# Performance work log

Measured on AMD Instinct MI355X. Metric: run time of the kernel, lower is better.

## Reference

```python
import jax, jax.numpy as jnp
import numpy as np
import math

N_HEAD = 16
ROPE_BASE = 10000.0

def _rope_cos_sin(seq_len, head_dim, dtype):
    inv_freq = 1.0 / (ROPE_BASE ** (jnp.arange(0, head_dim, 2, dtype=jnp.float32) / head_dim))
    t = jnp.arange(seq_len, dtype=jnp.float32)
    freqs = t[:, None] * inv_freq[None, :]            # [S, D/2]
    emb = jnp.concatenate([freqs, freqs], axis=-1)     # [S, D]
    # broadcast shape [1, 1, S, D] to match q/k [B, H, S, D]
    return jnp.cos(emb)[None, None].astype(dtype), jnp.sin(emb)[None, None].astype(dtype)

def _rotate_half(x):
    x1, x2 = jnp.split(x, 2, axis=-1)
    return jnp.concatenate([-x2, x1], axis=-1)

def setup_inputs() -> dict:
    key = jax.random.key(0)
    ks = jax.random.split(key, 5)
    B, S, E = 2, 2048, 1024
    x = jax.random.normal(ks[0], (B, S, E), dtype=jnp.float32)
    init = 1.0 / math.sqrt(E)
    Wq = jax.random.normal(ks[1], (E, E), dtype=jnp.float32) * init
    Wk = jax.random.normal(ks[2], (E, E), dtype=jnp.float32) * init
    Wv = jax.random.normal(ks[3], (E, E), dtype=jnp.float32) * init
    Wo = jax.random.normal(ks[4], (E, E), dtype=jnp.float32) * init
    # causal mask: True = masked (masked_fill with -inf)
    attn_mask = jnp.triu(jnp.ones((S, S), dtype=bool), k=1)
    return {"x": x, "Wq": Wq, "Wk": Wk, "Wv": Wv, "Wo": Wo, "attn_mask": attn_mask}

def reference(x, Wq, Wk, Wv, Wo, attn_mask):
    B, S, E = x.shape
    H = N_HEAD
    D = E // H
    # projections (torch Linear: y = x @ W.T), split heads -> [B, H, S, D]
    def proj(W):
        return jnp.einsum('bse,fe->bsf', x, W).reshape(B, S, H, D).transpose(0, 2, 1, 3)
    q, k, v = proj(Wq), proj(Wk), proj(Wv)
    cos, sin = _rope_cos_sin(S, D, x.dtype)
    q = q * cos + _rotate_half(q) * sin
    k = k * cos + _rotate_half(k) * sin
    scale = 1.0 / math.sqrt(D)
    scores = jnp.einsum('bhqd,bhkd->bhqk', q, k) * scale  # [B, H, S, S]
    scores = jnp.where(attn_mask[None, None], -jnp.inf, scores)
    attn = jax.nn.softmax(scores, axis=-1)
    out = jnp.einsum('bhqk,bhkd->bhqd', attn, v)           # [B, H, S, D]
    out = out.transpose(0, 2, 1, 3).reshape(B, S, E)
    return jnp.einsum('bse,fe->bsf', out, Wo)
```

## Files before the change

### kernel.cpp

```cpp
#include <hip/hip_runtime.h>
#include <hip/hip_bf16.h>

#define NB 2
#define NH 16
#define SEQ 2048
#define HD 64
#define EMB 1024

typedef unsigned short u16;
typedef unsigned int u32;
typedef __attribute__((ext_vector_type(8))) short bf16x8;
typedef __attribute__((ext_vector_type(4))) float f32x4;
typedef __attribute__((ext_vector_type(8))) unsigned short us8;

__device__ __forceinline__ float b2f(u16 u) {
    union { unsigned int i; float f; } v; v.i = ((unsigned int)u) << 16; return v.f;
}
__device__ __forceinline__ u16 f2b(float f) {
    union { float f; unsigned int i; } v; v.f = f;
    unsigned int x = v.i;
    return (u16)((x + 0x7FFFu + ((x >> 16) & 1u)) >> 16);
}
__device__ __forceinline__ u32 pk2(float a, float b) {
    union { __hip_bfloat162 h; u32 u; } v;
    v.h = __float22bfloat162_rn(make_float2(a, b));
    return v.u;
}

__device__ __forceinline__ void gld16(const u16* g, u16* l) {
    __builtin_amdgcn_global_load_lds((const __attribute__((address_space(1))) void*)g,
                                     (__attribute__((address_space(3))) void*)l, 16, 0, 0);
}

__global__ __launch_bounds__(256)
void detect_dtype_54571854463007(const u16* __restrict__ x, int* __restrict__ flag) {
    __shared__ int cnt;
    if (threadIdx.x == 0) cnt = 0;
    __syncthreads();
    const u16 v = x[threadIdx.x];
    const int e = (v >> 7) & 0xFF;
    if (e >= 110 && e <= 135) atomicAdd(&cnt, 1);
    __syncthreads();
    if (threadIdx.x == 0) *flag = (cnt >= 200) ? 1 : 0;
}

__device__ __forceinline__ void conv8(const void* src, u16* dst, int i, int isbf16) {
    if (isbf16) {
        *reinterpret_cast<uint4*>(dst + i) =
            *reinterpret_cast<const uint4*>((const u16*)src + i);
    } else {
        const float* s = (const float*)src + i;
        float4 a = *reinterpret_cast<const float4*>(s);
        float4 b = *reinterpret_cast<const float4*>(s + 4);
        us8 v;
        v[0] = f2b(a.x); v[1] = f2b(a.y); v[2] = f2b(a.z); v[3] = f2b(a.w);
        v[4] = f2b(b.x); v[5] = f2b(b.y); v[6] = f2b(b.z); v[7] = f2b(b.w);
        *reinterpret_cast<us8*>(dst + i) = v;
    }
}

__global__ __launch_bounds__(256)
void convert_54571854463007(const void* __restrict__ src, u16* __restrict__ dst,
                            const int* __restrict__ flagp, int n) {
    const int i = (blockIdx.x * 256 + threadIdx.x) * 8;
    if (i >= n) return;
    conv8(src, dst, i, *flagp);
}

__global__ __launch_bounds__(256)
void convertw_54571854463007(const void* __restrict__ w0, const void* __restrict__ w1,
                             const void* __restrict__ w2, const void* __restrict__ w3,
                             u16* __restrict__ dqkv, u16* __restrict__ dob,
                             const int* __restrict__ flagp) {
    const int NW = EMB * EMB;
    const int seg = blockIdx.y;
    const void* src = (seg == 0) ? w0 : (seg == 1) ? w1 : (seg == 2) ? w2 : w3;
    u16* dst = (seg < 3) ? (dqkv + (size_t)seg * NW) : dob;
    const int i = (blockIdx.x * 256 + threadIdx.x) * 8;
    conv8(src, dst, i, *flagp);
}

template<int OUT_MODE>
__global__ __launch_bounds__(256)
void gemm_mfma_54571854463007(const u16* __restrict__ A, const u16* __restrict__ Bw,
                              void* __restrict__ C, const int* __restrict__ flagp,
                              int M, int N, int K) {
    __shared__ __align__(16) u16 As[128 * 32];
    __shared__ __align__(16) u16 Bs[128 * 32];
    const int tid  = threadIdx.x;
    const int wave = tid >> 6, lane = tid & 63;
    const int quad = lane >> 4, fr = lane & 15;
    const int wr = (wave >> 1) * 64, wc = (wave & 1) * 64;
    const int m0 = blockIdx.y * 128, n0 = blockIdx.x * 128;
    const int r0 = tid >> 2;
    const int kc = (tid & 3) * 8;
    const f32x4 zz = {0.f, 0.f, 0.f, 0.f};
    f32x4 acc[4][4];
#pragma unroll
    for (int i = 0; i < 4; ++i)
#pragma unroll
        for (int j = 0; j < 4; ++j) acc[i][j] = zz;

    for (int k0 = 0; k0 < K; k0 += 32) {
        gld16(A  + (size_t)(m0 + r0) * K + k0 + kc,      &As[wave * 512]);
        gld16(A  + (size_t)(m0 + 64 + r0) * K + k0 + kc, &As[2048 + wave * 512]);
        gld16(Bw + (size_t)(n0 + r0) * K + k0 + kc,      &Bs[wave * 512]);
        gld16(Bw + (size_t)(n0 + 64 + r0) * K + k0 + kc, &Bs[2048 + wave * 512]);
        __syncthreads();
        bf16x8 af[4], bfr[4];
#pragma unroll
        for (int mi = 0; mi < 4; ++mi)
            af[mi] = *reinterpret_cast<const bf16x8*>(&As[(wr + mi * 16 + fr) * 32 + quad * 8]);
#pragma unroll
        for (int ni = 0; ni < 4; ++ni)
            bfr[ni] = *reinterpret_cast<const bf16x8*>(&Bs[(wc + ni * 16 + fr) * 32 + quad * 8]);
#pragma unroll
        for (int mi = 0; mi < 4; ++mi)
#pragma unroll
            for (int ni = 0; ni < 4; ++ni)
                acc[mi][ni] = __builtin_amdgcn_mfma_f32_16x16x32_bf16(af[mi], bfr[ni], acc[mi][ni], 0, 0, 0);
        __syncthreads();
    }

    if (OUT_MODE == 1) {
        const int t0 = n0 >> 10;
        if (t0 == 0) {
            const float SCL = 0.18033688011112042f;
#pragma unroll
            for (int mi = 0; mi < 4; ++mi)
#pragma unroll
                for (int ni = 0; ni < 4; ++ni)
#pragma unroll
                    for (int r = 0; r < 4; ++r) acc[mi][ni][r] *= SCL;
        }
        if (t0 < 2) {
            const float inv0 = __powf(10000.f, -(float)fr / 32.f);
            const float inv1 = __powf(10000.f, -(float)(fr + 16) / 32.f);
#pragma unroll
            for (int mi = 0; mi < 4; ++mi)
#pragma unroll
                for (int r = 0; r < 4; ++r) {
                    const int s = (m0 + wr + mi * 16 + quad * 4 + r) & (SEQ - 1);
#pragma unroll
                    for (int nl = 0; nl < 2; ++nl) {
                        float sn, cs;
                        __sincosf((float)s * (nl ? inv1 : inv0), &sn, &cs);
                        const float lo = acc[mi][nl][r], hi = acc[mi][nl + 2][r];
                        acc[mi][nl][r]     = lo * cs - hi * sn;
                        acc[mi][nl + 2][r] = hi * cs + lo * sn;
                    }
                }
        }
    }

    const int isbf16 = (OUT_MODE == 0) ? *flagp : 0;
    const size_t TS = (size_t)NB * NH * SEQ * HD;
#pragma unroll
    for (int mi = 0; mi < 4; ++mi)
#pragma unroll
        for (int ni = 0; ni < 4; ++ni)
#pragma unroll
            for (int r = 0; r < 4; ++r) {
                const int m = m0 + wr + mi * 16 + quad * 4 + r;
                const int n = n0 + wc + ni * 16 + fr;
                const float v = acc[mi][ni][r];
                if (OUT_MODE == 1) {
                    const int t = n >> 10, idx = n & 1023;
                    const int h = idx >> 6, d = idx & 63;
                    const int b = m >> 11, s = m & (SEQ - 1);
                    ((u16*)C)[t * TS + ((((size_t)b * NH + h) * SEQ + s) << 6) + d] = f2b(v);
                } else {
                    if (isbf16) ((u16*)C)[(size_t)m * N + n] = f2b(v);
                    else        ((float*)C)[(size_t)m * N + n] = v;
                }
            }
}

__device__ __forceinline__ void loadK_54571854463007(const u16* Kt, int fr, int quad,
                                                     bf16x8* kc) {
#pragma unroll
    for (int nt = 0; nt < 4; ++nt) {
        const u16* kp = Kt + (size_t)(nt * 16 + fr) * HD + quad * 8;
        kc[2 * nt]     = *reinterpret_cast<const bf16x8*>(kp);
        kc[2 * nt + 1] = *reinterpret_cast<const bf16x8*>(kp + 32);
    }
}

__global__ __launch_bounds__(256)
void flash_54571854463007(const u16* __restrict__ Q, const u16* __restrict__ K,
                          const u16* __restrict__ V, u16* __restrict__ AO) {
    __shared__ __align__(16) u16 Vt[2 * 4608];
    __shared__ __align__(16) u16 Ps[4608];
    const int tid  = threadIdx.x;
    const int w    = tid >> 6, lane = tid & 63;
    const int quad = lane >> 4, fr = lane & 15;
    const int qA = blockIdx.x;
    const int qB = 31 - qA;
    const int h = blockIdx.y, b = blockIdx.z;
    const size_t base = ((size_t)b * NH + h) * SEQ * HD;
    const int k2   = (tid & 31) * 2;
    const int key0 = (k2 & 3) * 16 + (k2 >> 2);
    const int d8   = ((tid >> 5) & 7) * 8;
    const int total = 33;

    const bf16x8 ones = {(short)0x3F80, (short)0x3F80, (short)0x3F80, (short)0x3F80,
                         (short)0x3F80, (short)0x3F80, (short)0x3F80, (short)0x3F80};

    const u16* qpA = Q + base + (size_t)(qA * 64 + w * 16 + fr) * HD + quad * 8;
    const u16* qpB = Q + base + (size_t)(qB * 64 + w * 16 + fr) * HD + quad * 8;
    const bf16x8 aqA0 = *reinterpret_cast<const bf16x8*>(qpA);
    const bf16x8 aqA1 = *reinterpret_cast<const bf16x8*>(qpA + 32);
    const bf16x8 aqB0 = *reinterpret_cast<const bf16x8*>(qpB);
    const bf16x8 aqB1 = *reinterpret_cast<const bf16x8*>(qpB + 32);

    bf16x8 kc[8], kn[8];
    loadK_54571854463007(K + base, fr, quad, kc);
    us8 vc0, vc1, vn0, vn1;
    {
        const u16* vs = V + base + (size_t)key0 * HD + d8;
        vc0 = *reinterpret_cast<const us8*>(vs);
        vc1 = *reinterpret_cast<const us8*>(vs + 16 * HD);
    }

    const f32x4 zz = {0.f, 0.f, 0.f, 0.f};
    f32x4 lacc = zz;
    f32x4 oacc[4];
#pragma unroll
    for (int nt = 0; nt < 4; ++nt) oacc[nt] = zz;

    for (int j = 0; j < total; ++j) {
        const int buf   = j & 1;
        const int phase = (j > qA) ? 1 : 0;
        const int qtile = phase ? qB : qA;
        const int kt    = phase ? (j - qA - 1) : j;
        const int vbase = buf * 4608;
#pragma unroll
        for (int jj = 0; jj < 8; ++jj) {
            const u32 pk = ((u32)(u16)vc1[jj] << 16) | (u32)(u16)vc0[jj];
            *reinterpret_cast<u32*>(&Vt[vbase + (d8 + jj) * 72 + k2]) = pk;
        }
        __syncthreads();
        if (j + 1 < total) {
            const int nkt = (j + 1 > qA) ? (j - qA) : (j + 1);
            loadK_54571854463007(K + base + (size_t)nkt * 64 * HD, fr, quad, kn);
            const u16* vs = V + base + (size_t)(nkt * 64 + key0) * HD + d8;
            vn0 = *reinterpret_cast<const us8*>(vs);
            vn1 = *reinterpret_cast<const us8*>(vs + 16 * HD);
        }
        const bf16x8 a0 = phase ? aqB0 : aqA0;
        const bf16x8 a1 = phase ? aqB1 : aqA1;
        f32x4 sa[4];
#pragma unroll
        for (int nt = 0; nt < 4; ++nt) {
            sa[nt] = __builtin_amdgcn_mfma_f32_16x16x32_bf16(a0, kc[2 * nt], zz, 0, 0, 0);
            sa[nt] = __builtin_amdgcn_mfma_f32_16x16x32_bf16(a1, kc[2 * nt + 1], sa[nt], 0, 0, 0);
        }
        if (kt == qtile) {
#pragma unroll
            for (int nt = 0; nt < 4; ++nt)
#pragma unroll
                for (int r = 0; r < 4; ++r)
                    if (nt * 16 + fr > w * 16 + quad * 4 + r) sa[nt][r] = -__builtin_inff();
        }
#pragma unroll
        for (int r = 0; r < 4; ++r) {
            const float p0 = exp2f(sa[0][r]);
            const float p1 = exp2f(sa[1][r]);
            const float p2 = exp2f(sa[2][r]);
            const float p3 = exp2f(sa[3][r]);
            *reinterpret_cast<uint2*>(&Ps[(w * 16 + quad * 4 + r) * 72 + 4 * fr]) =
                make_uint2(pk2(p0, p1), pk2(p2, p3));
        }
        bf16x8 ap0 = *reinterpret_cast<const bf16x8*>(&Ps[(w * 16 + fr) * 72 + quad * 8]);
        bf16x8 ap1 = *reinterpret_cast<const bf16x8*>(&Ps[(w * 16 + fr) * 72 + 32 + quad * 8]);
        lacc = __builtin_amdgcn_mfma_f32_16x16x32_bf16(ap0, ones, lacc, 0, 0, 0);
        lacc = __builtin_amdgcn_mfma_f32_16x16x32_bf16(ap1, ones, lacc, 0, 0, 0);
#pragma unroll
        for (int nt = 0; nt < 4; ++nt) {
            bf16x8 bv0 = *reinterpret_cast<const bf16x8*>(&Vt[vbase + (nt * 16 + fr) * 72 + quad * 8]);
            bf16x8 bv1 = *reinterpret_cast<const bf16x8*>(&Vt[vbase + (nt * 16 + fr) * 72 + 32 + quad * 8]);
            oacc[nt] = __builtin_amdgcn_mfma_f32_16x16x32_bf16(ap0, bv0, oacc[nt], 0, 0, 0);
            oacc[nt] = __builtin_amdgcn_mfma_f32_16x16x32_bf16(ap1, bv1, oacc[nt], 0, 0, 0);
        }
#pragma unroll
        for (int i = 0; i < 8; ++i) kc[i] = kn[i];
        vc0 = vn0; vc1 = vn1;
        if (j == qA || j == total - 1) {
#pragma unroll
            for (int r = 0; r < 4; ++r) {
                const float inv = 1.0f / lacc[r];
                const int q = qtile * 64 + w * 16 + quad * 4 + r;
#pragma unroll
                for (int nt = 0; nt < 4; ++nt)
                    AO[(((size_t)b * SEQ + q) * NH + h) * HD + nt * 16 + fr] = f2b(oacc[nt][r] * inv);
            }
            if (j == qA) {
                lacc = zz;
#pragma unroll
                for (int nt = 0; nt < 4; ++nt) oacc[nt] = zz;
            }
        }
    }
}

extern "C" void kernel_launch(void* const* d_in, const int* in_sizes, int n_in,
                              void* d_out, int out_size, void* d_ws, size_t ws_size,
                              hipStream_t stream) {
    (void)in_sizes; (void)n_in; (void)out_size; (void)ws_size;
    const void* x  = d_in[0];
    const void* Wq = d_in[1];
    const void* Wk = d_in[2];
    const void* Wv = d_in[3];
    const void* Wo = d_in[4];

    char* ws = (char*)d_ws;
    const size_t MB = 1024 * 1024;
    int* flag = (int*)ws;
    u16* xb   = (u16*)(ws + 64);
    u16* Wqkv = (u16*)(ws + 64 + 8 * MB);
    u16* Wob  = (u16*)(ws + 64 + 14 * MB);
    u16* Qb   = (u16*)(ws + 64 + 16 * MB);
    u16* Kb   = (u16*)(ws + 64 + 24 * MB);
    u16* Vb   = (u16*)(ws + 64 + 32 * MB);
    u16* AO   = xb;

    detect_dtype_54571854463007<<<1, 256, 0, stream>>>((const u16*)x, flag);

    const int NX = NB * SEQ * EMB;
    const int NW = EMB * EMB;
    convert_54571854463007<<<NX / 2048, 256, 0, stream>>>(x, xb, flag, NX);
    convertw_54571854463007<<<dim3(NW / 2048, 4), 256, 0, stream>>>(Wq, Wk, Wv, Wo, Wqkv, Wob, flag);

    const int M = NB * SEQ;
    gemm_mfma_54571854463007<1><<<dim3(3 * EMB / 128, M / 128), 256, 0, stream>>>(
        xb, Wqkv, Qb, flag, M, 3 * EMB, EMB);

    flash_54571854463007<<<dim3(16, NH, NB), 256, 0, stream>>>(Qb, Kb, Vb, AO);

    gemm_mfma_54571854463007<0><<<dim3(EMB / 128, M / 128), 256, 0, stream>>>(
        AO, Wob, d_out, flag, M, EMB, EMB);
}
```

Measured before the change: 240.4 us.

## Software-pipeline QK^T scores one tile ahead of softmax and PV in attention loop

Restructures the attention inner loop so the QK^T MFMA for tile j+1 is issued in iteration j, overlapping with the exp2/P-store and PV MFMAs of tile j. K loads are moved two tiles ahead to feed this. The aim is to hide MFMA latency and the exp/LDS dependency chain; in exchange it adds register pressure (extra score and K buffers), which could lower occupancy.

Measured after the change: 242.6 us. About the same (+0.9%).

```diff
diff --git a/kernel.cpp b/kernel.cpp
--- a/kernel.cpp
+++ b/kernel.cpp
@@ -213,16 +213,34 @@
     const bf16x8 aqB0 = *reinterpret_cast<const bf16x8*>(qpB);
     const bf16x8 aqB1 = *reinterpret_cast<const bf16x8*>(qpB + 32);
 
+    const f32x4 zz = {0.f, 0.f, 0.f, 0.f};
     bf16x8 kc[8], kn[8];
-    loadK_54571854463007(K + base, fr, quad, kc);
     us8 vc0, vc1, vn0, vn1;
+    f32x4 sa_cur[4], sa_next[4];
+
+    #define KTILE(i) (((i) <= qA) ? (i) : ((i) - qA - 1))
+
     {
+        bf16x8 k0[8];
+        loadK_54571854463007(K + base, fr, quad, k0);
         const u16* vs = V + base + (size_t)key0 * HD + d8;
         vc0 = *reinterpret_cast<const us8*>(vs);
         vc1 = *reinterpret_cast<const us8*>(vs + 16 * HD);
-    }
-
-    const f32x4 zz = {0.f, 0.f, 0.f, 0.f};
+        loadK_54571854463007(K + base + (size_t)KTILE(1) * 64 * HD, fr, quad, kc);
+#pragma unroll
+        for (int nt = 0; nt < 4; ++nt) {
+            sa_cur[nt] = __builtin_amdgcn_mfma_f32_16x16x32_bf16(aqA0, k0[2 * nt], zz, 0, 0, 0);
+            sa_cur[nt] = __builtin_amdgcn_mfma_f32_16x16x32_bf16(aqA1, k0[2 * nt + 1], sa_cur[nt], 0, 0, 0);
+        }
+        if (qA == 0) {
+#pragma unroll
+            for (int nt = 0; nt < 4; ++nt)
+#pragma unroll
+                for (int r = 0; r < 4; ++r)
+                    if (nt * 16 + fr > w * 16 + quad * 4 + r) sa_cur[nt][r] = -__builtin_inff();
+        }
+    }
+
     f32x4 lacc = zz;
     f32x4 oacc[4];
 #pragma unroll
@@ -230,9 +248,6 @@
 
     for (int j = 0; j < total; ++j) {
         const int buf   = j & 1;
-        const int phase = (j > qA) ? 1 : 0;
-        const int qtile = phase ? qB : qA;
-        const int kt    = phase ? (j - qA - 1) : j;
         const int vbase = buf * 4608;
 #pragma unroll
         for (int jj = 0; jj < 8; ++jj) {
@@ -240,34 +255,36 @@
             *reinterpret_cast<u32*>(&Vt[vbase + (d8 + jj) * 72 + k2]) = pk;
         }
         __syncthreads();
+        if (j + 2 < total)
+            loadK_54571854463007(K + base + (size_t)KTILE(j + 2) * 64 * HD, fr, quad, kn);
         if (j + 1 < total) {
-            const int nkt = (j + 1 > qA) ? (j - qA) : (j + 1);
-            loadK_54571854463007(K + base + (size_t)nkt * 64 * HD, fr, quad, kn);
-            const u16* vs = V + base + (size_t)(nkt * 64 + key0) * HD + d8;
+            const u16* vs = V + base + (size_t)(KTILE(j + 1) * 64 + key0) * HD + d8;
             vn0 = *reinterpret_cast<const us8*>(vs);
             vn1 = *reinterpret_cast<const us8*>(vs + 16 * HD);
         }
-        const bf16x8 a0 = phase ? aqB0 : aqA0;
-        const bf16x8 a1 = phase ? aqB1 : aqA1;
-        f32x4 sa[4];
-#pragma unroll
-        for (int nt = 0; nt < 4; ++nt) {
-            sa[nt] = __builtin_amdgcn_mfma_f32_16x16x32_bf16(a0, kc[2 * nt], zz, 0, 0, 0);
-            sa[nt] = __builtin_amdgcn_mfma_f32_16x16x32_bf16(a1, kc[2 * nt + 1], sa[nt], 0, 0, 0);
-        }
-        if (kt == qtile) {
-#pragma unroll
-            for (int nt = 0; nt < 4; ++nt)
-#pragma unroll
-                for (int r = 0; r < 4; ++r)
-                    if (nt * 16 + fr > w * 16 + quad * 4 + r) sa[nt][r] = -__builtin_inff();
+        if (j + 1 < total) {
+            const bool ph1 = (j + 1 > qA);
+            const bf16x8 a0 = ph1 ? aqB0 : aqA0;
+            const bf16x8 a1 = ph1 ? aqB1 : aqA1;
+#pragma unroll
+            for (int nt = 0; nt < 4; ++nt) {
+                sa_next[nt] = __builtin_amdgcn_mfma_f32_16x16x32_bf16(a0, kc[2 * nt], zz, 0, 0, 0);
+                sa_next[nt] = __builtin_amdgcn_mfma_f32_16x16x32_bf16(a1, kc[2 * nt + 1], sa_next[nt], 0, 0, 0);
+            }
+            if (j + 1 == qA || j + 1 == total - 1) {
+#pragma unroll
+                for (int nt = 0; nt < 4; ++nt)
+#pragma unroll
+                    for (int r = 0; r < 4; ++r)
+                        if (nt * 16 + fr > w * 16 + quad * 4 + r) sa_next[nt][r] = -__builtin_inff();
+            }
         }
 #pragma unroll
         for (int r = 0; r < 4; ++r) {
-            const float p0 = exp2f(sa[0][r]);
-            const float p1 = exp2f(sa[1][r]);
-            const float p2 = exp2f(sa[2][r]);
-            const float p3 = exp2f(sa[3][r]);
+            const float p0 = exp2f(sa_cur[0][r]);
+            const float p1 = exp2f(sa_cur[1][r]);
+            const float p2 = exp2f(sa_cur[2][r]);
+            const float p3 = exp2f(sa_cur[3][r]);
             *reinterpret_cast<uint2*>(&Ps[(w * 16 + quad * 4 + r) * 72 + 4 * fr]) =
                 make_uint2(pk2(p0, p1), pk2(p2, p3));
         }
@@ -283,9 +300,12 @@
             oacc[nt] = __builtin_amdgcn_mfma_f32_16x16x32_bf16(ap1, bv1, oacc[nt], 0, 0, 0);
         }
 #pragma unroll
+        for (int nt = 0; nt < 4; ++nt) sa_cur[nt] = sa_next[nt];
+#pragma unroll
         for (int i = 0; i < 8; ++i) kc[i] = kn[i];
         vc0 = vn0; vc1 = vn1;
         if (j == qA || j == total - 1) {
+            const int qtile = (j > qA) ? qB : qA;
 #pragma unroll
             for (int r = 0; r < 4; ++r) {
                 const float inv = 1.0f / lacc[r];
@@ -301,6 +321,7 @@
             }
         }
     }
+    #undef KTILE
 }
 
 extern "C" void kernel_launch(void* const* d_in, const int* in_sizes, int n_in,
```

## Split flash attention into single-wave blocks per 16-row quarter

Applied to the files above, without the earlier changes.

Launches the flash kernel as 2048 one-wave blocks, each owning a 16-row quarter of a paired causal q-tile. Each wave loads and transposes its own V tile into LDS without any block barrier, and the V double buffer and prefetch are removed. The intent is to drop __syncthreads stalls and raise occupancy with smaller LDS per block. The cost is fourfold redundant V loads and transposes, plus less latency hiding for V.

New measurement: 280.9 us. 16.9% more time.

```diff
diff --git a/kernel.cpp b/kernel.cpp
--- a/kernel.cpp
+++ b/kernel.cpp
@@ -186,41 +186,41 @@
     }
 }
 
-__global__ __launch_bounds__(256)
+__global__ __launch_bounds__(64, 2)
 void flash_54571854463007(const u16* __restrict__ Q, const u16* __restrict__ K,
                           const u16* __restrict__ V, u16* __restrict__ AO) {
-    __shared__ __align__(16) u16 Vt[2 * 4608];
-    __shared__ __align__(16) u16 Ps[4608];
-    const int tid  = threadIdx.x;
-    const int w    = tid >> 6, lane = tid & 63;
+    __shared__ __align__(16) u16 Vt[4608];
+    __shared__ __align__(16) u16 Ps[1152];
+    const int lane = threadIdx.x;
     const int quad = lane >> 4, fr = lane & 15;
-    const int qA = blockIdx.x;
-    const int qB = 31 - qA;
-    const int h = blockIdx.y, b = blockIdx.z;
+    const int lin  = blockIdx.x;
+    const int phb  = ((lin >> 5) << 3) | (lin & 7);
+    const int quarter = (lin >> 3) & 3;
+    const int p = phb & 15;
+    const int h = (phb >> 4) & 15;
+    const int b = phb >> 8;
+    const int qA = p, qB = 31 - p;
+    const int ro = quarter * 16;
     const size_t base = ((size_t)b * NH + h) * SEQ * HD;
-    const int k2   = (tid & 31) * 2;
-    const int key0 = (k2 & 3) * 16 + (k2 >> 2);
-    const int d8   = ((tid >> 5) & 7) * 8;
+    const int k2    = (lane & 31) * 2;
+    const int key0  = (k2 & 3) * 16 + (k2 >> 2);
+    const int dbase = (lane >> 5) * 32;
     const int total = 33;
 
     const bf16x8 ones = {(short)0x3F80, (short)0x3F80, (short)0x3F80, (short)0x3F80,
                          (short)0x3F80, (short)0x3F80, (short)0x3F80, (short)0x3F80};
 
-    const u16* qpA = Q + base + (size_t)(qA * 64 + w * 16 + fr) * HD + quad * 8;
-    const u16* qpB = Q + base + (size_t)(qB * 64 + w * 16 + fr) * HD + quad * 8;
+    const u16* qpA = Q + base + (size_t)(qA * 64 + ro + fr) * HD + quad * 8;
+    const u16* qpB = Q + base + (size_t)(qB * 64 + ro + fr) * HD + quad * 8;
     const bf16x8 aqA0 = *reinterpret_cast<const bf16x8*>(qpA);
     const bf16x8 aqA1 = *reinterpret_cast<const bf16x8*>(qpA + 32);
     const bf16x8 aqB0 = *reinterpret_cast<const bf16x8*>(qpB);
     const bf16x8 aqB1 = *reinterpret_cast<const bf16x8*>(qpB + 32);
 
+    #define KTILE(i) (((i) <= qA) ? (i) : ((i) - qA - 1))
+
     bf16x8 kc[8], kn[8];
     loadK_54571854463007(K + base, fr, quad, kc);
-    us8 vc0, vc1, vn0, vn1;
-    {
-        const u16* vs = V + base + (size_t)key0 * HD + d8;
-        vc0 = *reinterpret_cast<const us8*>(vs);
-        vc1 = *reinterpret_cast<const us8*>(vs + 16 * HD);
-    }
 
     const f32x4 zz = {0.f, 0.f, 0.f, 0.f};
     f32x4 lacc = zz;
@@ -229,29 +229,23 @@
     for (int nt = 0; nt < 4; ++nt) oacc[nt] = zz;
 
     for (int j = 0; j < total; ++j) {
-        const int buf   = j & 1;
-        const int phase = (j > qA) ? 1 : 0;
+        const int phase = (j > qA);
         const int qtile = phase ? qB : qA;
         const int kt    = phase ? (j - qA - 1) : j;
-        const int vbase = buf * 4608;
-#pragma unroll
-        for (int jj = 0; jj < 8; ++jj) {
-            const u32 pk = ((u32)(u16)vc1[jj] << 16) | (u32)(u16)vc0[jj];
-            *reinterpret_cast<u32*>(&Vt[vbase + (d8 + jj) * 72 + k2]) = pk;
-        }
-        __syncthreads();
-        if (j + 1 < total) {
-            const int nkt = (j + 1 > qA) ? (j - qA) : (j + 1);
-            loadK_54571854463007(K + base + (size_t)nkt * 64 * HD, fr, quad, kn);
-            const u16* vs = V + base + (size_t)(nkt * 64 + key0) * HD + d8;
-            vn0 = *reinterpret_cast<const us8*>(vs);
-            vn1 = *reinterpret_cast<const us8*>(vs + 16 * HD);
-        }
-        const bf16x8 a0 = phase ? aqB0 : aqA0;
-        const bf16x8 a1 = phase ? aqB1 : aqA1;
+        const u16* vs = V + base + (size_t)(kt * 64 + key0) * HD + dbase;
+        us8 va[4], vb[4];
+#pragma unroll
+        for (int i = 0; i < 4; ++i) {
+            va[i] = *reinterpret_cast<const us8*>(vs + i * 8);
+            vb[i] = *reinterpret_cast<const us8*>(vs + 16 * HD + i * 8);
+        }
+        if (j + 1 < total)
+            loadK_54571854463007(K + base + (size_t)KTILE(j + 1) * 64 * HD, fr, quad, kn);
         f32x4 sa[4];
 #pragma unroll
         for (int nt = 0; nt < 4; ++nt) {
+            const bf16x8 a0 = phase ? aqB0 : aqA0;
+            const bf16x8 a1 = phase ? aqB1 : aqA1;
             sa[nt] = __builtin_amdgcn_mfma_f32_16x16x32_bf16(a0, kc[2 * nt], zz, 0, 0, 0);
             sa[nt] = __builtin_amdgcn_mfma_f32_16x16x32_bf16(a1, kc[2 * nt + 1], sa[nt], 0, 0, 0);
         }
@@ -260,7 +254,7 @@
             for (int nt = 0; nt < 4; ++nt)
 #pragma unroll
                 for (int r = 0; r < 4; ++r)
-                    if (nt * 16 + fr > w * 16 + quad * 4 + r) sa[nt][r] = -__builtin_inff();
+                    if (nt * 16 + fr > ro + quad * 4 + r) sa[nt][r] = -__builtin_inff();
         }
 #pragma unroll
         for (int r = 0; r < 4; ++r) {
@@ -268,28 +262,34 @@
             const float p1 = exp2f(sa[1][r]);
             const float p2 = exp2f(sa[2][r]);
             const float p3 = exp2f(sa[3][r]);
-            *reinterpret_cast<uint2*>(&Ps[(w * 16 + quad * 4 + r) * 72 + 4 * fr]) =
+            *reinterpret_cast<uint2*>(&Ps[(quad * 4 + r) * 72 + 4 * fr]) =
                 make_uint2(pk2(p0, p1), pk2(p2, p3));
         }
-        bf16x8 ap0 = *reinterpret_cast<const bf16x8*>(&Ps[(w * 16 + fr) * 72 + quad * 8]);
-        bf16x8 ap1 = *reinterpret_cast<const bf16x8*>(&Ps[(w * 16 + fr) * 72 + 32 + quad * 8]);
+#pragma unroll
+        for (int i = 0; i < 4; ++i)
+#pragma unroll
+            for (int jj = 0; jj < 8; ++jj) {
+                const u32 pk = ((u32)(u16)vb[i][jj] << 16) | (u32)(u16)va[i][jj];
+                *reinterpret_cast<u32*>(&Vt[(dbase + i * 8 + jj) * 72 + k2]) = pk;
+            }
+        const bf16x8 ap0 = *reinterpret_cast<const bf16x8*>(&Ps[fr * 72 + quad * 8]);
+        const bf16x8 ap1 = *reinterpret_cast<const bf16x8*>(&Ps[fr * 72 + 32 + quad * 8]);
         lacc = __builtin_amdgcn_mfma_f32_16x16x32_bf16(ap0, ones, lacc, 0, 0, 0);
         lacc = __builtin_amdgcn_mfma_f32_16x16x32_bf16(ap1, ones, lacc, 0, 0, 0);
 #pragma unroll
         for (int nt = 0; nt < 4; ++nt) {
-            bf16x8 bv0 = *reinterpret_cast<const bf16x8*>(&Vt[vbase + (nt * 16 + fr) * 72 + quad * 8]);
-            bf16x8 bv1 = *reinterpret_cast<const bf16x8*>(&Vt[vbase + (nt * 16 + fr) * 72 + 32 + quad * 8]);
+            const bf16x8 bv0 = *reinterpret_cast<const bf16x8*>(&Vt[(nt * 16 + fr) * 72 + quad * 8]);
+            const bf16x8 bv1 = *reinterpret_cast<const bf16x8*>(&Vt[(nt * 16 + fr) * 72 + 32 + quad * 8]);
             oacc[nt] = __builtin_amdgcn_mfma_f32_16x16x32_bf16(ap0, bv0, oacc[nt], 0, 0, 0);
             oacc[nt] = __builtin_amdgcn_mfma_f32_16x16x32_bf16(ap1, bv1, oacc[nt], 0, 0, 0);
         }
 #pragma unroll
         for (int i = 0; i < 8; ++i) kc[i] = kn[i];
-        vc0 = vn0; vc1 = vn1;
         if (j == qA || j == total - 1) {
 #pragma unroll
             for (int r = 0; r < 4; ++r) {
                 const float inv = 1.0f / lacc[r];
-                const int q = qtile * 64 + w * 16 + quad * 4 + r;
+                const int q = qtile * 64 + ro + quad * 4 + r;
 #pragma unroll
                 for (int nt = 0; nt < 4; ++nt)
                     AO[(((size_t)b * SEQ + q) * NH + h) * HD + nt * 16 + fr] = f2b(oacc[nt][r] * inv);
@@ -301,6 +301,7 @@
             }
         }
     }
+    #undef KTILE
 }
 
 extern "C" void kernel_launch(void* const* d_in, const int* in_sizes, int n_in,
@@ -335,7 +336,7 @@
     gemm_mfma_54571854463007<1><<<dim3(3 * EMB / 128, M / 128), 256, 0, stream>>>(
         xb, Wqkv, Qb, flag, M, 3 * EMB, EMB);
 
-    flash_54571854463007<<<dim3(16, NH, NB), 256, 0, stream>>>(Qb, Kb, Vb, AO);
+    flash_54571854463007<<<dim3(2048), 64, 0, stream>>>(Qb, Kb, Vb, AO);
 
     gemm_mfma_54571854463007<0><<<dim3(EMB / 128, M / 128), 256, 0, stream>>>(
         AO, Wob, d_out, flag, M, EMB, EMB);
```
